# Performance work log

Measured on AMD Instinct MI355X. Metric: run time of the kernel, lower is better.

The kernel has to match this reference:

```python
import jax, jax.numpy as jnp
import numpy as np

GAMMA = 1.0
INF_REPLACE = 1e10  # original code replaces inf with 1e10 before logsumexp


def _softmin3(r_diag, r_up, r_left, gamma):
    # softmin over the 3 DP neighbors (stack order matches original: diag, up, left)
    x = jnp.stack([r_diag, r_up, r_left], axis=0)  # (3, B)
    x = jnp.where(jnp.isinf(x), jnp.asarray(INF_REPLACE, x.dtype), x)
    return -gamma * jax.nn.logsumexp(-x / gamma, axis=0)  # (B,)


def _cdist(X, Y):
    # Euclidean pairwise distance, torch.cdist(p=2): (B,N,d),(B,M,d) -> (B,N,M)
    d2 = (jnp.sum(X * X, axis=-1)[:, :, None]
          + jnp.sum(Y * Y, axis=-1)[:, None, :]
          - 2.0 * jnp.einsum('bnd,bmd->bnm', X, Y))
    return jnp.sqrt(jnp.maximum(d2, 0.0))


def _soft_dtw(X, Y, gamma):
    B, N, _ = X.shape
    D = _cdist(X, Y)  # (B, N, N)
    inf = jnp.asarray(jnp.inf, D.dtype)

    # R row 0: [0, inf, inf, ...] per batch
    prev_row0 = jnp.full((B, N + 1), inf, dtype=D.dtype).at[:, 0].set(0.0)

    def row_step(prev_row, d_row):
        # prev_row: (B, N+1) = R[i-1, :]; d_row: (B, N) = D[:, i-1, :]
        xs = (d_row.T, prev_row[:, :-1].T, prev_row[:, 1:].T)  # each (N, B)

        def col_step(r_left, x):
            d, r_diag, r_up = x  # each (B,)
            r = d + _softmin3(r_diag, r_up, r_left, gamma)
            return r, r

        _, row = jax.lax.scan(col_step, jnp.full((B,), inf, dtype=D.dtype), xs)
        new_row = jnp.concatenate([jnp.full((B, 1), inf, dtype=D.dtype), row.T], axis=1)
        return new_row, None

    last_row, _ = jax.lax.scan(row_step, prev_row0, jnp.swapaxes(D, 0, 1))
    return last_row[:, -1]  # R[:, N, N], shape (B,)


def setup_inputs() -> dict:
    key = jax.random.key(0)
    kx, ky = jax.random.split(key)
    B, N, d = 64, 512, 64
    X = jax.random.normal(kx, (B, N, d), dtype=jnp.float32)
    Y = jax.random.normal(ky, (B, N, d), dtype=jnp.float32)
    return {"X": X, "Y": Y}


def reference(X, Y):
    return _soft_dtw(X, Y, GAMMA)
```

## Files before the change

### kernel.cpp

```cpp
#include <hip/hip_runtime.h>
#include <math.h>

#define NB 64
#define NN 512
#define ND 64

#define LOG2E 1.4426950408889634f
#define LN2   0.6931471805599453f
#define RING  12
#define NINF  __int_as_float(0xFF800000u)

typedef __attribute__((ext_vector_type(8))) short  bf16x8;
typedef __attribute__((ext_vector_type(4))) float  f32x4;

static __device__ __forceinline__ unsigned short f2bf(float f) {
    unsigned u = __float_as_uint(f);
    u += 0x7FFFu + ((u >> 16) & 1u);
    return (unsigned short)(u >> 16);
}

__global__ __launch_bounds__(256) void cdist_kernel(const float* __restrict__ X,
                                                    const float* __restrict__ Y,
                                                    unsigned short* __restrict__ Wt) {
    __shared__ float nxs[128];
    __shared__ float nys[128];

    const int b  = blockIdx.z;
    const int ib = blockIdx.x * 128;
    const int jb = blockIdx.y * 128;
    const int t  = threadIdx.x;

    {
        const int r = t & 127;
        const float* src = (t < 128)
            ? (X + ((size_t)b * NN + ib + r) * ND)
            : (Y + ((size_t)b * NN + jb + r) * ND);
        float s = 0.f;
        #pragma unroll
        for (int k = 0; k < ND; k += 4) {
            float4 v = *(const float4*)(src + k);
            s += v.x * v.x + v.y * v.y + v.z * v.z + v.w * v.w;
        }
        if (t < 128) nxs[r] = s; else nys[r] = s;
    }
    __syncthreads();

    const int wave = t >> 6;
    const int wi   = (wave & 1) * 64;
    const int wj   = (wave >> 1) * 64;
    const int lane = t & 63;
    const int lm   = lane & 15;
    const int quad = lane >> 4;

    f32x4 acc[4][4];
    #pragma unroll
    for (int mt = 0; mt < 4; ++mt)
        #pragma unroll
        for (int nt = 0; nt < 4; ++nt)
            acc[mt][nt] = (f32x4){0.f, 0.f, 0.f, 0.f};

    #pragma unroll
    for (int h = 0; h < 2; ++h) {
        bf16x8 Af[4], Bf[4];
        #pragma unroll
        for (int mt = 0; mt < 4; ++mt) {
            const float* p = Y + ((size_t)b * NN + jb + wj + mt * 16 + lm) * ND
                               + h * 32 + quad * 8;
            float4 v0 = *(const float4*)p;
            float4 v1 = *(const float4*)(p + 4);
            bf16x8 a;
            a[0] = f2bf(v0.x); a[1] = f2bf(v0.y); a[2] = f2bf(v0.z); a[3] = f2bf(v0.w);
            a[4] = f2bf(v1.x); a[5] = f2bf(v1.y); a[6] = f2bf(v1.z); a[7] = f2bf(v1.w);
            Af[mt] = a;
        }
        #pragma unroll
        for (int nt = 0; nt < 4; ++nt) {
            const float* p = X + ((size_t)b * NN + ib + wi + nt * 16 + lm) * ND
                               + h * 32 + quad * 8;
            float4 v0 = *(const float4*)p;
            float4 v1 = *(const float4*)(p + 4);
            bf16x8 a;
            a[0] = f2bf(v0.x); a[1] = f2bf(v0.y); a[2] = f2bf(v0.z); a[3] = f2bf(v0.w);
            a[4] = f2bf(v1.x); a[5] = f2bf(v1.y); a[6] = f2bf(v1.z); a[7] = f2bf(v1.w);
            Bf[nt] = a;
        }
        #pragma unroll
        for (int mt = 0; mt < 4; ++mt)
            #pragma unroll
            for (int nt = 0; nt < 4; ++nt)
                acc[mt][nt] = __builtin_amdgcn_mfma_f32_16x16x32_bf16(
                    Af[mt], Bf[nt], acc[mt][nt], 0, 0, 0);
    }

    float nxv[4], nyv[4][4];
    #pragma unroll
    for (int nt = 0; nt < 4; ++nt) nxv[nt] = nxs[wi + nt * 16 + lm];
    #pragma unroll
    for (int mt = 0; mt < 4; ++mt)
        #pragma unroll
        for (int r = 0; r < 4; ++r) nyv[mt][r] = nys[wj + mt * 16 + quad * 4 + r];

    #pragma unroll
    for (int mt = 0; mt < 4; ++mt) {
        const int j = jb + wj + mt * 16 + quad * 4;
        unsigned short* Drow = Wt + ((size_t)b * NN + j) * NN + ib + wi + lm;
        #pragma unroll
        for (int r = 0; r < 4; ++r) {
            #pragma unroll
            for (int nt = 0; nt < 4; ++nt) {
                float d2 = nyv[mt][r] + nxv[nt] - 2.0f * acc[mt][nt][r];
                float w  = __builtin_amdgcn_exp2f(16.0f - LOG2E * sqrtf(fmaxf(d2, 0.f)));
                Drow[(size_t)r * NN + nt * 16] = f2bf(w);
            }
        }
    }
}

static __device__ __forceinline__ void dtw_step(
    bool DOACT, bool DOGUARD, bool DOREN, bool DOCLAMP,
    int ss, int u, int t, const unsigned short* __restrict__ Wb, int ib,
    uint4* ring, float* L, float& diagHold, float& h, float& Otf)
{
    const float recvH = __int_as_float(__builtin_amdgcn_update_dpp(
        (int)0xFF800000, __float_as_int(h), 0x138 , 0xf, 0xf, false));

    if (DOACT) { if (ss == t && t > 0) Otf = -recvH; }

    const float up0   = __builtin_amdgcn_exp2f(fminf(recvH + Otf, 80.0f));
    const float diag0 = diagHold;
    diagHold = up0 * 65536.0f;

    const int j = ss - t + 1;
    const uint4 c = ring[u];

    {
        int jn = j + RING;
        if (DOCLAMP) jn = jn < 1 ? 1 : jn;
        ring[u] = *(const uint4*)(Wb + (size_t)(jn - 1) * NN + ib);
    }

    bool act = true;
    if (DOGUARD) act = (j >= 1) && (j <= NN);
    if (act) {
        float dd[8];
        dd[0] = __uint_as_float(c.x << 16);
        dd[1] = __uint_as_float(c.x & 0xFFFF0000u);
        dd[2] = __uint_as_float(c.y << 16);
        dd[3] = __uint_as_float(c.y & 0xFFFF0000u);
        dd[4] = __uint_as_float(c.z << 16);
        dd[5] = __uint_as_float(c.z & 0xFFFF0000u);
        dd[6] = __uint_as_float(c.w << 16);
        dd[7] = __uint_as_float(c.w & 0xFFFF0000u);

        float pre[8], cc[8];
        pre[0] = diag0 + L[0];
        #pragma unroll
        for (int k = 1; k < 8; ++k)
            pre[k] = fmaf(65536.0f, L[k - 1], L[k]);
        #pragma unroll
        for (int k = 0; k < 8; ++k) cc[k] = dd[k] * pre[k];
        float r = up0;
        #pragma unroll
        for (int k = 0; k < 8; ++k) {
            r = fmaf(dd[k], r, cc[k]);
            L[k] = r;
        }

        if (DOREN) {
            float m8 = fmaxf(fmaxf(fmaxf(L[0], L[1]), fmaxf(L[2], L[3])),
                             fmaxf(fmaxf(L[4], L[5]), fmaxf(L[6], L[7])));
            const int   e  = (int)(__float_as_uint(m8) >> 23) - 127;
            const float sc = __uint_as_float((unsigned)(127 - e) << 23);
            #pragma unroll
            for (int k = 0; k < 8; ++k) L[k] *= sc;
            diagHold *= sc;
            Otf -= (float)e;
        }

        h = __builtin_amdgcn_logf(L[7]) - Otf;
    }
}

__global__ __launch_bounds__(64) void dtw_kernel(const unsigned short* __restrict__ Wt,
                                                 float* __restrict__ out) {
    const int b = blockIdx.x;
    const int t = threadIdx.x;
    const unsigned short* __restrict__ Wb = Wt + (size_t)b * NN * NN;
    const int ib = 8 * t;

    float L[8];
    #pragma unroll
    for (int k = 0; k < 8; ++k) L[k] = 0.0f;

    float diagHold = (t == 0) ? 65536.0f : 0.0f;
    float h        = NINF;
    float Otf      = 0.0f;

    uint4 ring[RING];
    #pragma unroll
    for (int u = 0; u < RING; ++u) {
        int col = u - t + 1;
        col = col < 1 ? 1 : col;
        ring[u] = *(const uint4*)(Wb + (size_t)(col - 1) * NN + ib);
    }

    for (int sb = 0; sb < 72; sb += RING)
        #pragma unroll
        for (int u = 0; u < RING; ++u)
            dtw_step(true, true, (u & 1) == 1, true,
                     sb + u, u, t, Wb, ib, ring, L, diagHold, h, Otf);

    for (int sb = 72; sb < 504; sb += RING)
        #pragma unroll
        for (int u = 0; u < RING; ++u)
            dtw_step(false, false, (u & 1) == 1, false,
                     sb + u, u, t, Wb, ib, ring, L, diagHold, h, Otf);

    for (int sb = 504; sb < 576; sb += RING)
        #pragma unroll
        for (int u = 0; u < RING; ++u)
            dtw_step(false, true, (u & 1) == 1, false,
                     sb + u, u, t, Wb, ib, ring, L, diagHold, h, Otf);

    if (t == 63) out[b] = (16384.0f - h) * LN2;
}

extern "C" void kernel_launch(void* const* d_in, const int* in_sizes, int n_in,
                              void* d_out, int out_size, void* d_ws, size_t ws_size,
                              hipStream_t stream) {
    const float* X = (const float*)d_in[0];
    const float* Y = (const float*)d_in[1];
    float* out = (float*)d_out;
    unsigned short* Wt = (unsigned short*)d_ws;

    cdist_kernel<<<dim3(4, 4, NB), 256, 0, stream>>>(X, Y, Wt);
    dtw_kernel<<<NB, 64, 0, stream>>>(Wt, out);
}
```

Before: 165.1 us.

## Pre-pack X/Y into MFMA-fragment bf16 layout with precomputed norms

Adds a pack kernel that converts X and Y to bf16 once, lays them out in the exact per-lane MFMA fragment order, and computes row squared norms into workspace. The cdist kernel then loads contiguous bf16x8 fragments and norms directly, dropping the redundant fp32 reloads, per-block norm recompute, conversions and the shared-memory sync. This adds an extra kernel launch and a workspace round trip, while the dominant serial DTW kernel is unchanged.

```diff
diff --git a/kernel.cpp b/kernel.cpp
--- a/kernel.cpp
+++ b/kernel.cpp
@@ -19,31 +19,59 @@
     return (unsigned short)(u >> 16);
 }
 
-__global__ __launch_bounds__(256) void cdist_kernel(const float* __restrict__ X,
-                                                    const float* __restrict__ Y,
+__global__ __launch_bounds__(256) void pack_kernel(const float* __restrict__ X,
+                                                   const float* __restrict__ Y,
+                                                   unsigned short* __restrict__ Xp,
+                                                   unsigned short* __restrict__ Yp,
+                                                   float* __restrict__ nx,
+                                                   float* __restrict__ ny) {
+    const int gid = blockIdx.x * 256 + threadIdx.x;
+    const float* src;
+    unsigned short* dst;
+    float* ndst;
+    if (blockIdx.y == 0) { src = X + (size_t)gid * ND; dst = Xp; ndst = nx; }
+    else                 { src = Y + (size_t)gid * ND; dst = Yp; ndst = ny; }
+
+    float v[ND];
+    float s = 0.f;
+    #pragma unroll
+    for (int k = 0; k < ND; k += 4) {
+        float4 f = *(const float4*)(src + k);
+        v[k] = f.x; v[k + 1] = f.y; v[k + 2] = f.z; v[k + 3] = f.w;
+        s += f.x * f.x + f.y * f.y + f.z * f.z + f.w * f.w;
+    }
+    ndst[gid] = s;
+
+    const int b  = gid >> 9;
+    const int i  = gid & 511;
+    const int it = i >> 4;
+    const int lm = i & 15;
+    #pragma unroll
+    for (int h = 0; h < 2; ++h) {
+        #pragma unroll
+        for (int q = 0; q < 4; ++q) {
+            unsigned w[4];
+            #pragma unroll
+            for (int m = 0; m < 4; ++m) {
+                const int c = h * 32 + q * 8 + 2 * m;
+                w[m] = (unsigned)f2bf(v[c]) | ((unsigned)f2bf(v[c + 1]) << 16);
+            }
+            uint4 pkt; pkt.x = w[0]; pkt.y = w[1]; pkt.z = w[2]; pkt.w = w[3];
+            *(uint4*)(dst + ((((size_t)b * 32 + it) * 2 + h) << 9)
+                          + (size_t)(q * 16 + lm) * 8) = pkt;
+        }
+    }
+}
+
+__global__ __launch_bounds__(256) void cdist_kernel(const unsigned short* __restrict__ Xp,
+                                                    const unsigned short* __restrict__ Yp,
+                                                    const float* __restrict__ nx,
+                                                    const float* __restrict__ ny,
                                                     unsigned short* __restrict__ Wt) {
-    __shared__ float nxs[128];
-    __shared__ float nys[128];
-
     const int b  = blockIdx.z;
     const int ib = blockIdx.x * 128;
     const int jb = blockIdx.y * 128;
     const int t  = threadIdx.x;
-
-    {
-        const int r = t & 127;
-        const float* src = (t < 128)
-            ? (X + ((size_t)b * NN + ib + r) * ND)
-            : (Y + ((size_t)b * NN + jb + r) * ND);
-        float s = 0.f;
-        #pragma unroll
-        for (int k = 0; k < ND; k += 4) {
-            float4 v = *(const float4*)(src + k);
-            s += v.x * v.x + v.y * v.y + v.z * v.z + v.w * v.w;
-        }
-        if (t < 128) nxs[r] = s; else nys[r] = s;
-    }
-    __syncthreads();
 
     const int wave = t >> 6;
     const int wi   = (wave & 1) * 64;
@@ -59,31 +87,20 @@
         for (int nt = 0; nt < 4; ++nt)
             acc[mt][nt] = (f32x4){0.f, 0.f, 0.f, 0.f};
 
+    const int jt0 = (jb + wj) >> 4;
+    const int it0 = (ib + wi) >> 4;
+
     #pragma unroll
     for (int h = 0; h < 2; ++h) {
         bf16x8 Af[4], Bf[4];
         #pragma unroll
-        for (int mt = 0; mt < 4; ++mt) {
-            const float* p = Y + ((size_t)b * NN + jb + wj + mt * 16 + lm) * ND
-                               + h * 32 + quad * 8;
-            float4 v0 = *(const float4*)p;
-            float4 v1 = *(const float4*)(p + 4);
-            bf16x8 a;
-            a[0] = f2bf(v0.x); a[1] = f2bf(v0.y); a[2] = f2bf(v0.z); a[3] = f2bf(v0.w);
-            a[4] = f2bf(v1.x); a[5] = f2bf(v1.y); a[6] = f2bf(v1.z); a[7] = f2bf(v1.w);
-            Af[mt] = a;
-        }
-        #pragma unroll
-        for (int nt = 0; nt < 4; ++nt) {
-            const float* p = X + ((size_t)b * NN + ib + wi + nt * 16 + lm) * ND
-                               + h * 32 + quad * 8;
-            float4 v0 = *(const float4*)p;
-            float4 v1 = *(const float4*)(p + 4);
-            bf16x8 a;
-            a[0] = f2bf(v0.x); a[1] = f2bf(v0.y); a[2] = f2bf(v0.z); a[3] = f2bf(v0.w);
-            a[4] = f2bf(v1.x); a[5] = f2bf(v1.y); a[6] = f2bf(v1.z); a[7] = f2bf(v1.w);
-            Bf[nt] = a;
-        }
+        for (int mt = 0; mt < 4; ++mt)
+            Af[mt] = *(const bf16x8*)(Yp
+                + ((((size_t)b * 32 + jt0 + mt) * 2 + h) << 9) + (size_t)lane * 8);
+        #pragma unroll
+        for (int nt = 0; nt < 4; ++nt)
+            Bf[nt] = *(const bf16x8*)(Xp
+                + ((((size_t)b * 32 + it0 + nt) * 2 + h) << 9) + (size_t)lane * 8);
         #pragma unroll
         for (int mt = 0; mt < 4; ++mt)
             #pragma unroll
@@ -94,11 +111,13 @@
 
     float nxv[4], nyv[4][4];
     #pragma unroll
-    for (int nt = 0; nt < 4; ++nt) nxv[nt] = nxs[wi + nt * 16 + lm];
+    for (int nt = 0; nt < 4; ++nt)
+        nxv[nt] = nx[(size_t)b * NN + ib + wi + nt * 16 + lm];
     #pragma unroll
     for (int mt = 0; mt < 4; ++mt)
         #pragma unroll
-        for (int r = 0; r < 4; ++r) nyv[mt][r] = nys[wj + mt * 16 + quad * 4 + r];
+        for (int r = 0; r < 4; ++r)
+            nyv[mt][r] = ny[(size_t)b * NN + jb + wj + mt * 16 + quad * 4 + r];
 
     #pragma unroll
     for (int mt = 0; mt < 4; ++mt) {
@@ -231,8 +250,15 @@
     const float* X = (const float*)d_in[0];
     const float* Y = (const float*)d_in[1];
     float* out = (float*)d_out;
-    unsigned short* Wt = (unsigned short*)d_ws;
-
-    cdist_kernel<<<dim3(4, 4, NB), 256, 0, stream>>>(X, Y, Wt);
+
+    char* ws = (char*)d_ws;
+    unsigned short* Wt = (unsigned short*)(ws);
+    unsigned short* Xp = (unsigned short*)(ws + (33554432));
+    unsigned short* Yp = (unsigned short*)(ws + (33554432 + 4194304));
+    float* nx = (float*)(ws + (33554432 + 2 * 4194304));
+    float* ny = (float*)(ws + (33554432 + 2 * 4194304 + 131072));
+
+    pack_kernel<<<dim3(NB * NN / 256, 2), 256, 0, stream>>>(X, Y, Xp, Yp, nx, ny);
+    cdist_kernel<<<dim3(4, 4, NB), 256, 0, stream>>>(Xp, Yp, nx, ny, Wt);
     dtw_kernel<<<NB, 64, 0, stream>>>(Wt, out);
 }
```

Result: faster. 153.0 us (-7.3%).
